# Kernel tuning notes

Measured on AMD Instinct MI355X. Metric: run time of the kernel, lower is better.

## Reference

```python
import jax, jax.numpy as jnp
import numpy as np

B, N, C, H, HD, HH, WW, K, ALPHA = 8, 4096, 256, 8, 32, 64, 64, 5, 4.0


def setup_inputs() -> dict:
    key = jax.random.key(0)
    ks = jax.random.split(key, 6)
    return {
        "x": jax.random.normal(ks[0], (B, N, C), jnp.float32),
        "W_qg": jax.random.normal(ks[1], (C, 2 * C), jnp.float32) * 0.02,
        "W_kv": jax.random.normal(ks[2], (C, 2 * C), jnp.float32) * 0.02,
        "W_proj": jax.random.normal(ks[3], (C, C), jnp.float32) * 0.02,
        "b_proj": jnp.zeros((C,), jnp.float32),
        "dwc_w": jax.random.normal(ks[4], (HD, 1, K, K), jnp.float32) * 0.05,
        "dwc_b": jnp.zeros((HD,), jnp.float32),
        "power_p": jnp.zeros((1, H, 1, HD), jnp.float32),
    }


def _safe_pow(x, p):
    # x >= 0 (post-relu). 0**p == 0 for p > 0; guard base so grads stay finite.
    xs = jnp.where(x > 0, x, 1.0)
    return jnp.where(x > 0, xs ** p, 0.0)


def reference(x, W_qg, W_kv, W_proj, b_proj, dwc_w, dwc_b, power_p):
    qg = x @ W_qg                                  # (B,N,2C)
    q, g = qg[..., :C], qg[..., C:]
    kv = x @ W_kv                                  # (B,N,2C)
    k = kv[..., :C].reshape(B, N, H, HD).transpose(0, 2, 1, 3)   # (B,H,N,hd)
    v = kv[..., C:].reshape(B, N, H, HD).transpose(0, 2, 1, 3)
    q = q.reshape(B, N, H, HD).transpose(0, 2, 1, 3)

    power = 1.0 + ALPHA * jax.nn.sigmoid(power_p)  # (1,H,1,hd)
    # x_s = q_pos@kv_s + q_neg@kv_s = (q_pos+q_neg)@kv_s, kv_s = (k_pos+k_neg)^T v_s
    q_sum = _safe_pow(jax.nn.relu(q), power) + _safe_pow(jax.nn.relu(-q), power)
    k_sum = _safe_pow(jax.nn.relu(k), power) + _safe_pow(jax.nn.relu(-k), power)

    v_s, v_o = v[..., : HD // 2], v[..., HD // 2 :]
    kv_s = jnp.einsum('bhnd,bhne->bhde', k_sum, v_s)
    kv_o = jnp.einsum('bhnd,bhne->bhde', k_sum, v_o)
    x_s = jnp.einsum('bhnd,bhde->bhne', q_sum, kv_s)
    x_o = jnp.einsum('bhnd,bhde->bhne', q_sum, kv_o)
    x_att = jnp.concatenate([x_s, x_o], -1).transpose(0, 2, 1, 3).reshape(B, N, C)

    # depthwise conv branch: exact layout replication of torch permute/reshape chain
    v_img = v.transpose(0, 2, 1, 3).reshape(B * H, HD, HH, WW)
    pad = K // 2
    v_loc = jax.lax.conv_general_dilated(
        v_img, dwc_w, (1, 1), [(pad, pad), (pad, pad)],
        feature_group_count=HD,
        dimension_numbers=('NCHW', 'OIHW', 'NCHW')) + dwc_b[None, :, None, None]
    v_loc = v_loc.reshape(B, H, HD, N).transpose(0, 2, 1, 3).reshape(B, C, N).transpose(0, 2, 1)

    return ((x_att + v_loc) * g) @ W_proj + b_proj
```

## Files before the change

kernel.cpp:

```cpp
#include <hip/hip_runtime.h>
#include <hip/hip_bf16.h>
#include <math.h>

#define B_ 8
#define N_ 4096
#define C_ 256
#define H_ 8
#define HD_ 32
#define BN_ (B_ * N_)
#define E_ ((size_t)BN_ * C_)

typedef __attribute__((ext_vector_type(8))) short short8;
typedef __attribute__((ext_vector_type(4))) float f32x4;

__device__ __forceinline__ float b2f(__hip_bfloat16 x) { return __bfloat162float(x); }

__device__ __forceinline__ void gl_lds16(const void* gp, void* lp) {
    __builtin_amdgcn_global_load_lds(
        (const __attribute__((address_space(1))) unsigned int*)gp,
        (__attribute__((address_space(3))) unsigned int*)lp,
        16, 0, 0);
}

__device__ __forceinline__ float fast_abspow(float v, float p) {
    float av = fabsf(v);
    return (av > 0.f) ? exp2f(p * __log2f(av)) : 0.f;
}

__device__ __forceinline__ float bf_lo(unsigned u) { return __uint_as_float(u << 16); }
__device__ __forceinline__ float bf_hi(unsigned u) { return __uint_as_float(u & 0xffff0000u); }
__device__ __forceinline__ unsigned short f2bfbits(float f) {
    __hip_bfloat16 h = __float2bfloat16(f);
    return *(unsigned short*)&h;
}

__global__ __launch_bounds__(256) void cvt_all(
    const float* __restrict__ x, const float* __restrict__ Wqg,
    const float* __restrict__ Wkv, const float* __restrict__ Wp,
    const float* __restrict__ pp,
    __hip_bfloat16* __restrict__ xb, __hip_bfloat16* __restrict__ Wt1,
    __hip_bfloat16* __restrict__ Wt2, float* __restrict__ powers)
{
    int t = threadIdx.x;
    int bid0 = blockIdx.x;
    if (bid0 < 8192) {
        size_t i = ((size_t)bid0 * 256 + t) * 4;
        float4 v = *(const float4*)&x[i];
        xb[i + 0] = __float2bfloat16(v.x);
        xb[i + 1] = __float2bfloat16(v.y);
        xb[i + 2] = __float2bfloat16(v.z);
        xb[i + 3] = __float2bfloat16(v.w);
        return;
    }
    int bid = bid0 - 8192;
    if (bid == 80) {
        powers[t] = 1.0f + 4.0f / (1.0f + expf(-pp[t]));
        return;
    }
    __shared__ float tile[64][65];
    const float* src;
    __hip_bfloat16* dst;
    int scols, tr, tc, dn0;
    if (bid < 32)      { src = Wqg; scols = 512; tr = bid >> 3;        tc = bid & 7;        dst = Wt1; dn0 = tc * 64; }
    else if (bid < 64) { src = Wkv; scols = 512; tr = (bid - 32) >> 3; tc = (bid - 32) & 7; dst = Wt1; dn0 = 512 + tc * 64; }
    else               { src = Wp;  scols = 256; tr = (bid - 64) >> 2; tc = (bid - 64) & 3; dst = Wt2; dn0 = tc * 64; }
    int tx = t & 63, ty = t >> 6;
    #pragma unroll
    for (int i = 0; i < 16; i++) {
        int r = ty + i * 4;
        tile[r][tx] = src[(size_t)(tr * 64 + r) * scols + tc * 64 + tx];
    }
    __syncthreads();
    #pragma unroll
    for (int i = 0; i < 16; i++) {
        int n_local = ty + i * 4;
        dst[(size_t)(dn0 + n_local) * 256 + tr * 64 + tx] = __float2bfloat16(tile[tx][n_local]);
    }
}

__global__ __launch_bounds__(256) void gemm1_mfma(
    const __hip_bfloat16* __restrict__ xb, const __hip_bfloat16* __restrict__ Wt1,
    const float* __restrict__ powers,
    __hip_bfloat16* __restrict__ q16, __hip_bfloat16* __restrict__ k16,
    __hip_bfloat16* __restrict__ g16, __hip_bfloat16* __restrict__ v16)
{
    __shared__ __align__(16) unsigned short As[2 * 128 * 32];
    __shared__ __align__(16) unsigned short Bs[2 * 128 * 32];
    int t = threadIdx.x;
    int w = t >> 6, l = t & 63;
    int row0 = blockIdx.x * 128;
    int col0 = blockIdx.y * 128;
    int wm = (w >> 1) * 64, wn = (w & 1) * 64;
    int lane15 = l & 15, quad = l >> 4;
    int srow = l >> 2;
    int skcol = (l & 3) * 8;

    f32x4 acc[4][4];
    #pragma unroll
    for (int mi = 0; mi < 4; mi++)
        #pragma unroll
        for (int ni = 0; ni < 4; ni++) acc[mi][ni] = (f32x4){0.f, 0.f, 0.f, 0.f};

    for (int k0 = 0; k0 < 256; k0 += 64) {
        #pragma unroll
        for (int kh = 0; kh < 2; kh++) {
            #pragma unroll
            for (int i = 0; i < 2; i++) {
                int r = i * 64 + w * 16 + srow;
                int kc = k0 + kh * 32 + skcol;
                gl_lds16(&xb[(size_t)(row0 + r) * 256 + kc],
                         &As[kh * 4096 + (i * 64 + w * 16) * 32]);
                gl_lds16(&Wt1[(size_t)(col0 + r) * 256 + kc],
                         &Bs[kh * 4096 + (i * 64 + w * 16) * 32]);
            }
        }
        __syncthreads();
        #pragma unroll
        for (int kh = 0; kh < 2; kh++) {
            short8 a[4], b[4];
            #pragma unroll
            for (int mi = 0; mi < 4; mi++)
                a[mi] = *(const short8*)&As[kh * 4096 + (wm + mi * 16 + lane15) * 32 + quad * 8];
            #pragma unroll
            for (int ni = 0; ni < 4; ni++)
                b[ni] = *(const short8*)&Bs[kh * 4096 + (wn + ni * 16 + lane15) * 32 + quad * 8];
            #pragma unroll
            for (int mi = 0; mi < 4; mi++)
                #pragma unroll
                for (int ni = 0; ni < 4; ni++)
                    acc[mi][ni] = __builtin_amdgcn_mfma_f32_16x16x32_bf16(a[mi], b[ni], acc[mi][ni], 0, 0, 0);
        }
        __syncthreads();
    }

    int region = blockIdx.y >> 1;
    #pragma unroll
    for (int mi = 0; mi < 4; mi++) {
        #pragma unroll
        for (int ni = 0; ni < 4; ni++) {
            int row = row0 + wm + mi * 16 + quad * 4;
            int col = col0 + wn + ni * 16 + lane15;
            int c255 = col & 255;
            float p = powers[c255];
            #pragma unroll
            for (int r = 0; r < 4; r++) {
                float v = acc[mi][ni][r];
                size_t idx = (size_t)(row + r) * 256 + c255;
                if (region == 0) {
                    q16[idx] = __float2bfloat16(fast_abspow(v, p));
                } else if (region == 1) {
                    g16[idx] = __float2bfloat16(v);
                } else if (region == 2) {
                    k16[idx] = __float2bfloat16(fast_abspow(v, p));
                } else {
                    v16[idx] = __float2bfloat16(v);
                }
            }
        }
    }
}

__global__ __launch_bounds__(256) void kvmat_kernel(
    const __hip_bfloat16* __restrict__ k16, const __hip_bfloat16* __restrict__ v16,
    float* __restrict__ kv_part)
{
    __shared__ __align__(16) unsigned short Kl[16 * 256];
    __shared__ __align__(16) unsigned short Vl[16 * 256];
    int t = threadIdx.x;
    int bid = blockIdx.x;
    int b = bid >> 5, seg = bid & 31;
    int h = t >> 5;
    float acc[32];
    #pragma unroll
    for (int e = 0; e < 32; e++) acc[e] = 0.f;
    const size_t base = (size_t)b * N_ * 256;
    int row = t >> 4, colb = (t & 15) * 16;
    for (int n0 = seg * 128; n0 < seg * 128 + 128; n0 += 16) {
        const uint4* ks = (const uint4*)(k16 + base + (size_t)(n0 + row) * 256 + colb);
        uint4 ka = ks[0], kb = ks[1];
        const uint4* vs = (const uint4*)(v16 + base + (size_t)(n0 + row) * 256 + colb);
        uint4 va = vs[0], vb = vs[1];
        __syncthreads();
        uint4* kd4 = (uint4*)&Kl[row * 256 + colb];
        kd4[0] = ka; kd4[1] = kb;
        uint4* vd4 = (uint4*)&Vl[row * 256 + colb];
        vd4[0] = va; vd4[1] = vb;
        __syncthreads();
        #pragma unroll
        for (int nn = 0; nn < 16; nn++) {
            unsigned short ku = Kl[nn * 256 + t];
            float kd = bf_lo((unsigned)ku);
            const uint4* vp = (const uint4*)&Vl[nn * 256 + h * 32];
            uint4 v0 = vp[0], v1 = vp[1], v2 = vp[2], v3 = vp[3];
            unsigned us[16] = {v0.x, v0.y, v0.z, v0.w, v1.x, v1.y, v1.z, v1.w,
                               v2.x, v2.y, v2.z, v2.w, v3.x, v3.y, v3.z, v3.w};
            #pragma unroll
            for (int j = 0; j < 16; j++) {
                acc[2 * j]     += kd * bf_lo(us[j]);
                acc[2 * j + 1] += kd * bf_hi(us[j]);
            }
        }
    }
    float* dst = kv_part + (size_t)bid * 8192;
    #pragma unroll
    for (int e = 0; e < 32; e++) dst[e * 256 + t] = acc[e];
}

__global__ __launch_bounds__(256) void kv_reduce(
    const float* __restrict__ kv_part, float* __restrict__ kv_mat2)
{
    int bid = blockIdx.x, t = threadIdx.x;
    int b = bid >> 3, chunk = bid & 7;
    #pragma unroll
    for (int j = 0; j < 4; j++) {
        int i = chunk * 1024 + j * 256 + t;
        float s = 0.f;
        for (int seg = 0; seg < 32; seg++)
            s += kv_part[((size_t)b * 32 + seg) * 8192 + i];
        kv_mat2[(size_t)b * 8192 + i] = s;
    }
}

__global__ __launch_bounds__(256) void conv_kernel(
    const __hip_bfloat16* __restrict__ v16,
    const float* __restrict__ w, const float* __restrict__ bias,
    __hip_bfloat16* __restrict__ vloc)
{
    __shared__ __align__(16) float img[64 * 72];
    __shared__ float wl[25];
    int t = threadIdx.x;
    int gid = blockIdx.x;
    int DD = gid & 31;
    if (t < 128) {
        int row = t >> 1, side = (t & 1) * 68;
        *(float4*)&img[row * 72 + side] = (float4){0.f, 0.f, 0.f, 0.f};
    }
    if (t < 25) wl[t] = w[DD * 25 + t];
    {
        int row = t >> 2, colb = (t & 3) * 16;
        const uint4* src = (const uint4*)(v16 + (size_t)gid * 4096 + row * 64 + colb);
        uint4 u0 = src[0], u1 = src[1];
        float4* d = (float4*)&img[row * 72 + 4 + colb];
        d[0] = (float4){bf_lo(u0.x), bf_hi(u0.x), bf_lo(u0.y), bf_hi(u0.y)};
        d[1] = (float4){bf_lo(u0.z), bf_hi(u0.z), bf_lo(u0.w), bf_hi(u0.w)};
        d[2] = (float4){bf_lo(u1.x), bf_hi(u1.x), bf_lo(u1.y), bf_hi(u1.y)};
        d[3] = (float4){bf_lo(u1.z), bf_hi(u1.z), bf_lo(u1.w), bf_hi(u1.w)};
    }
    __syncthreads();
    float bs = bias[DD];
    int x0 = (t & 15) * 4, yb = t >> 4;
    #pragma unroll
    for (int s = 0; s < 4; s++) {
        int y = yb + s * 16;
        float a0 = bs, a1 = bs, a2 = bs, a3 = bs;
        #pragma unroll
        for (int ky = 0; ky < 5; ky++) {
            int row = y + ky - 2;
            if (row < 0 || row >= 64) continue;
            const float* rp = &img[row * 72 + x0];
            float4 w0 = *(const float4*)rp;
            float4 w1 = *(const float4*)(rp + 4);
            float4 w2 = *(const float4*)(rp + 8);
            float win[12] = {w0.x, w0.y, w0.z, w0.w, w1.x, w1.y, w1.z, w1.w,
                             w2.x, w2.y, w2.z, w2.w};
            #pragma unroll
            for (int kx = 0; kx < 5; kx++) {
                float wt = wl[ky * 5 + kx];
                a0 += wt * win[2 + kx];
                a1 += wt * win[3 + kx];
                a2 += wt * win[4 + kx];
                a3 += wt * win[5 + kx];
            }
        }
        unsigned lo = (unsigned)f2bfbits(a0) | ((unsigned)f2bfbits(a1) << 16);
        unsigned hi = (unsigned)f2bfbits(a2) | ((unsigned)f2bfbits(a3) << 16);
        *(uint2*)(vloc + (size_t)gid * 4096 + y * 64 + x0) = (uint2){lo, hi};
    }
}

#define A2P 264
__global__ __launch_bounds__(256) void att_gemm2(
    const __hip_bfloat16* __restrict__ q16, const float* __restrict__ kv_mat2,
    const __hip_bfloat16* __restrict__ vloc, const __hip_bfloat16* __restrict__ g16,
    const __hip_bfloat16* __restrict__ Wt2, const float* __restrict__ bp,
    float* __restrict__ out)
{
    __shared__ __align__(16) unsigned short QA[64 * A2P];
    __shared__ __align__(16) unsigned short Bs[256 * 32];
    int t = threadIdx.x;
    int w = t >> 6, l = t & 63;
    int r0 = blockIdx.x * 64;
    int b = r0 >> 12, n0 = r0 & 4095;
    int lane15 = l & 15, quad = l >> 4;
    int h0 = w * 2;

    {
        const uint4* qsrc = (const uint4*)(q16 + (size_t)(r0 + (t >> 2)) * 256 + (t & 3) * 64);
        uint4* qdst = (uint4*)&QA[(t >> 2) * A2P + (t & 3) * 64];
        #pragma unroll
        for (int j = 0; j < 8; j++) qdst[j] = qsrc[j];
    }
    __syncthreads();

    short8 afr[4][2];
    #pragma unroll
    for (int m = 0; m < 4; m++)
        #pragma unroll
        for (int hh = 0; hh < 2; hh++)
            afr[m][hh] = *(const short8*)&QA[(m * 16 + lane15) * A2P + (h0 + hh) * 32 + quad * 8];

    short8 bfr[2][2];
    #pragma unroll
    for (int hh = 0; hh < 2; hh++) {
        #pragma unroll
        for (int nt = 0; nt < 2; nt++) {
            const float4* kp = (const float4*)(kv_mat2 + (size_t)b * 8192 +
                (size_t)(nt * 16 + lane15) * 256 + (h0 + hh) * 32 + quad * 8);
            float4 ka = kp[0], kb = kp[1];
            short8 bb;
            bb[0] = (short)f2bfbits(ka.x); bb[1] = (short)f2bfbits(ka.y);
            bb[2] = (short)f2bfbits(ka.z); bb[3] = (short)f2bfbits(ka.w);
            bb[4] = (short)f2bfbits(kb.x); bb[5] = (short)f2bfbits(kb.y);
            bb[6] = (short)f2bfbits(kb.z); bb[7] = (short)f2bfbits(kb.w);
            bfr[hh][nt] = bb;
        }
    }

    f32x4 ac[4][2][2];
    #pragma unroll
    for (int m = 0; m < 4; m++)
        #pragma unroll
        for (int hh = 0; hh < 2; hh++)
            #pragma unroll
            for (int nt = 0; nt < 2; nt++)
                ac[m][hh][nt] = __builtin_amdgcn_mfma_f32_16x16x32_bf16(
                    afr[m][hh], bfr[hh][nt], (f32x4){0.f, 0.f, 0.f, 0.f}, 0, 0, 0);

    #pragma unroll
    for (int m = 0; m < 4; m++) {
        #pragma unroll
        for (int hh = 0; hh < 2; hh++) {
            #pragma unroll
            for (int nt = 0; nt < 2; nt++) {
                int col = (h0 + hh) * 32 + nt * 16 + lane15;
                int rowb = m * 16 + quad * 4;
                size_t img = ((size_t)((b * 8 + (col & 7)) * 32 + (col >> 3))) * 4096 + n0 + rowb;
                uint2 vv = *(const uint2*)(vloc + img);
                float vl[4] = {bf_lo(vv.x), bf_hi(vv.x), bf_lo(vv.y), bf_hi(vv.y)};
                #pragma unroll
                for (int i = 0; i < 4; i++) {
                    float gg = b2f(g16[(size_t)(r0 + rowb + i) * 256 + col]);
                    float val = (ac[m][hh][nt][i] + vl[i]) * gg;
                    QA[(rowb + i) * A2P + col] = f2bfbits(val);
                }
            }
        }
    }

    int wm = (w & 1) * 32, wn = (w >> 1) * 128;
    f32x4 acc2[2][8];
    #pragma unroll
    for (int mi = 0; mi < 2; mi++)
        #pragma unroll
        for (int ni = 0; ni < 8; ni++) acc2[mi][ni] = (f32x4){0.f, 0.f, 0.f, 0.f};

    for (int k0 = 0; k0 < 256; k0 += 32) {
        __syncthreads();
        #pragma unroll
        for (int i = 0; i < 4; i++) {
            int ncol = i * 64 + w * 16 + (l >> 2);
            gl_lds16(&Wt2[(size_t)ncol * 256 + k0 + (l & 3) * 8],
                     &Bs[(i * 64 + w * 16) * 32]);
        }
        __syncthreads();
        short8 a[2], bb[8];
        #pragma unroll
        for (int mi = 0; mi < 2; mi++)
            a[mi] = *(const short8*)&QA[(wm + mi * 16 + lane15) * A2P + k0 + quad * 8];
        #pragma unroll
        for (int ni = 0; ni < 8; ni++)
            bb[ni] = *(const short8*)&Bs[(wn + ni * 16 + lane15) * 32 + quad * 8];
        #pragma unroll
        for (int mi = 0; mi < 2; mi++)
            #pragma unroll
            for (int ni = 0; ni < 8; ni++)
                acc2[mi][ni] = __builtin_amdgcn_mfma_f32_16x16x32_bf16(a[mi], bb[ni], acc2[mi][ni], 0, 0, 0);
    }

    #pragma unroll
    for (int mi = 0; mi < 2; mi++) {
        #pragma unroll
        for (int ni = 0; ni < 8; ni++) {
            int row = r0 + wm + mi * 16 + quad * 4;
            int col = wn + ni * 16 + lane15;
            float bv = bp[col];
            #pragma unroll
            for (int r = 0; r < 4; r++)
                out[(size_t)(row + r) * 256 + col] = acc2[mi][ni][r] + bv;
        }
    }
}

extern "C" void kernel_launch(void* const* d_in, const int* in_sizes, int n_in,
                              void* d_out, int out_size, void* d_ws, size_t ws_size,
                              hipStream_t stream) {
    const float* x      = (const float*)d_in[0];
    const float* W_qg   = (const float*)d_in[1];
    const float* W_kv   = (const float*)d_in[2];
    const float* W_proj = (const float*)d_in[3];
    const float* b_proj = (const float*)d_in[4];
    const float* dwc_w  = (const float*)d_in[5];
    const float* dwc_b  = (const float*)d_in[6];
    const float* pow_p  = (const float*)d_in[7];
    float* out = (float*)d_out;

    float* ws = (float*)d_ws;
    const size_t E = E_;
    __hip_bfloat16* q16  = (__hip_bfloat16*)ws;
    __hip_bfloat16* k16  = (__hip_bfloat16*)(ws + E / 2);
    __hip_bfloat16* vl16 = k16;
    __hip_bfloat16* g16  = (__hip_bfloat16*)(ws + E);
    __hip_bfloat16* v16  = (__hip_bfloat16*)(ws + 3 * E / 2);
    __hip_bfloat16* xb   = (__hip_bfloat16*)(ws + 2 * E);
    float* kv_part = ws + 5 * E / 2;
    float* kv_mat2 = kv_part + 256 * 8192;
    __hip_bfloat16* Wt1 = (__hip_bfloat16*)(kv_mat2 + 65536);
    __hip_bfloat16* Wt2 = Wt1 + 262144;
    float* powers = (float*)(Wt2 + 65536);

    cvt_all<<<8192 + 81, 256, 0, stream>>>(x, W_qg, W_kv, W_proj, pow_p, xb, Wt1, Wt2, powers);
    gemm1_mfma<<<dim3(BN_ / 128, 8), 256, 0, stream>>>(xb, Wt1, powers, q16, k16, g16, v16);
    kvmat_kernel<<<256, 256, 0, stream>>>(k16, v16, kv_part);
    kv_reduce<<<64, 256, 0, stream>>>(kv_part, kv_mat2);
    conv_kernel<<<2048, 256, 0, stream>>>(v16, dwc_w, dwc_b, vl16);
    att_gemm2<<<512, 256, 0, stream>>>(q16, kv_mat2, vl16, g16, Wt2, b_proj, out);
}
```

Before: 206.6 us.

## Stage GEMM1 epilogue through LDS and fuse kv-matrix, reduction and conv kernels

The GEMM1 epilogue now writes results into a padded shared-memory tile and then stores them to global memory as coalesced 16-byte rows, replacing scattered 2-byte stores. The kv-matrix kernel, kv reduction kernel and depthwise conv kernel are merged into one launch with heterogeneous blocks. Partial kv sums are combined with float atomicAdd into a buffer zeroed by a memset, which removes the separate reduction pass. The conv output moves to its own workspace region because k16 is still being read concurrently, and the atomics make the float summation order nondeterministic.

```diff
diff --git a/kernel.cpp b/kernel.cpp
--- a/kernel.cpp
+++ b/kernel.cpp
@@ -78,14 +78,16 @@
     }
 }
 
+#define EP 132
 __global__ __launch_bounds__(256) void gemm1_mfma(
     const __hip_bfloat16* __restrict__ xb, const __hip_bfloat16* __restrict__ Wt1,
     const float* __restrict__ powers,
     __hip_bfloat16* __restrict__ q16, __hip_bfloat16* __restrict__ k16,
     __hip_bfloat16* __restrict__ g16, __hip_bfloat16* __restrict__ v16)
 {
-    __shared__ __align__(16) unsigned short As[2 * 128 * 32];
-    __shared__ __align__(16) unsigned short Bs[2 * 128 * 32];
+    __shared__ __align__(16) unsigned short SMEM[128 * EP];
+    unsigned short* As = SMEM;
+    unsigned short* Bs = SMEM + 8192;
     int t = threadIdx.x;
     int w = t >> 6, l = t & 63;
     int row0 = blockIdx.x * 128;
@@ -134,147 +136,129 @@
     }
 
     int region = blockIdx.y >> 1;
+    bool dopow = (region == 0) || (region == 2);
     #pragma unroll
     for (int mi = 0; mi < 4; mi++) {
         #pragma unroll
         for (int ni = 0; ni < 4; ni++) {
-            int row = row0 + wm + mi * 16 + quad * 4;
-            int col = col0 + wn + ni * 16 + lane15;
-            int c255 = col & 255;
-            float p = powers[c255];
+            int lrow = wm + mi * 16 + quad * 4;
+            int lcol = wn + ni * 16 + lane15;
+            float p = powers[(col0 + lcol) & 255];
             #pragma unroll
             for (int r = 0; r < 4; r++) {
                 float v = acc[mi][ni][r];
-                size_t idx = (size_t)(row + r) * 256 + c255;
-                if (region == 0) {
-                    q16[idx] = __float2bfloat16(fast_abspow(v, p));
-                } else if (region == 1) {
-                    g16[idx] = __float2bfloat16(v);
-                } else if (region == 2) {
-                    k16[idx] = __float2bfloat16(fast_abspow(v, p));
-                } else {
-                    v16[idx] = __float2bfloat16(v);
-                }
+                float o = dopow ? fast_abspow(v, p) : v;
+                SMEM[(lrow + r) * EP + lcol] = f2bfbits(o);
             }
         }
     }
-}
-
-__global__ __launch_bounds__(256) void kvmat_kernel(
+    __syncthreads();
+    __hip_bfloat16* dst = (region == 0) ? q16 : (region == 1) ? g16 : (region == 2) ? k16 : v16;
+    int sr = t >> 1, sc = (t & 1) * 64;
+    const unsigned short* src = &SMEM[sr * EP + sc];
+    __hip_bfloat16* gp = dst + (size_t)(row0 + sr) * 256 + ((col0 + sc) & 255);
+    #pragma unroll
+    for (int j = 0; j < 8; j++)
+        *(uint4*)(gp + j * 8) = *(const uint4*)(src + j * 8);
+}
+
+__global__ __launch_bounds__(256) void kvmat_conv(
     const __hip_bfloat16* __restrict__ k16, const __hip_bfloat16* __restrict__ v16,
-    float* __restrict__ kv_part)
-{
-    __shared__ __align__(16) unsigned short Kl[16 * 256];
-    __shared__ __align__(16) unsigned short Vl[16 * 256];
-    int t = threadIdx.x;
-    int bid = blockIdx.x;
-    int b = bid >> 5, seg = bid & 31;
-    int h = t >> 5;
-    float acc[32];
-    #pragma unroll
-    for (int e = 0; e < 32; e++) acc[e] = 0.f;
-    const size_t base = (size_t)b * N_ * 256;
-    int row = t >> 4, colb = (t & 15) * 16;
-    for (int n0 = seg * 128; n0 < seg * 128 + 128; n0 += 16) {
-        const uint4* ks = (const uint4*)(k16 + base + (size_t)(n0 + row) * 256 + colb);
-        uint4 ka = ks[0], kb = ks[1];
-        const uint4* vs = (const uint4*)(v16 + base + (size_t)(n0 + row) * 256 + colb);
-        uint4 va = vs[0], vb = vs[1];
-        __syncthreads();
-        uint4* kd4 = (uint4*)&Kl[row * 256 + colb];
-        kd4[0] = ka; kd4[1] = kb;
-        uint4* vd4 = (uint4*)&Vl[row * 256 + colb];
-        vd4[0] = va; vd4[1] = vb;
-        __syncthreads();
-        #pragma unroll
-        for (int nn = 0; nn < 16; nn++) {
-            unsigned short ku = Kl[nn * 256 + t];
-            float kd = bf_lo((unsigned)ku);
-            const uint4* vp = (const uint4*)&Vl[nn * 256 + h * 32];
-            uint4 v0 = vp[0], v1 = vp[1], v2 = vp[2], v3 = vp[3];
-            unsigned us[16] = {v0.x, v0.y, v0.z, v0.w, v1.x, v1.y, v1.z, v1.w,
-                               v2.x, v2.y, v2.z, v2.w, v3.x, v3.y, v3.z, v3.w};
-            #pragma unroll
-            for (int j = 0; j < 16; j++) {
-                acc[2 * j]     += kd * bf_lo(us[j]);
-                acc[2 * j + 1] += kd * bf_hi(us[j]);
-            }
-        }
-    }
-    float* dst = kv_part + (size_t)bid * 8192;
-    #pragma unroll
-    for (int e = 0; e < 32; e++) dst[e * 256 + t] = acc[e];
-}
-
-__global__ __launch_bounds__(256) void kv_reduce(
-    const float* __restrict__ kv_part, float* __restrict__ kv_mat2)
-{
-    int bid = blockIdx.x, t = threadIdx.x;
-    int b = bid >> 3, chunk = bid & 7;
-    #pragma unroll
-    for (int j = 0; j < 4; j++) {
-        int i = chunk * 1024 + j * 256 + t;
-        float s = 0.f;
-        for (int seg = 0; seg < 32; seg++)
-            s += kv_part[((size_t)b * 32 + seg) * 8192 + i];
-        kv_mat2[(size_t)b * 8192 + i] = s;
-    }
-}
-
-__global__ __launch_bounds__(256) void conv_kernel(
-    const __hip_bfloat16* __restrict__ v16,
+    float* __restrict__ kv_mat2,
     const float* __restrict__ w, const float* __restrict__ bias,
     __hip_bfloat16* __restrict__ vloc)
 {
-    __shared__ __align__(16) float img[64 * 72];
-    __shared__ float wl[25];
+    __shared__ __align__(16) float SM[4640];
     int t = threadIdx.x;
-    int gid = blockIdx.x;
-    int DD = gid & 31;
-    if (t < 128) {
-        int row = t >> 1, side = (t & 1) * 68;
-        *(float4*)&img[row * 72 + side] = (float4){0.f, 0.f, 0.f, 0.f};
-    }
-    if (t < 25) wl[t] = w[DD * 25 + t];
-    {
-        int row = t >> 2, colb = (t & 3) * 16;
-        const uint4* src = (const uint4*)(v16 + (size_t)gid * 4096 + row * 64 + colb);
-        uint4 u0 = src[0], u1 = src[1];
-        float4* d = (float4*)&img[row * 72 + 4 + colb];
-        d[0] = (float4){bf_lo(u0.x), bf_hi(u0.x), bf_lo(u0.y), bf_hi(u0.y)};
-        d[1] = (float4){bf_lo(u0.z), bf_hi(u0.z), bf_lo(u0.w), bf_hi(u0.w)};
-        d[2] = (float4){bf_lo(u1.x), bf_hi(u1.x), bf_lo(u1.y), bf_hi(u1.y)};
-        d[3] = (float4){bf_lo(u1.z), bf_hi(u1.z), bf_lo(u1.w), bf_hi(u1.w)};
-    }
-    __syncthreads();
-    float bs = bias[DD];
-    int x0 = (t & 15) * 4, yb = t >> 4;
-    #pragma unroll
-    for (int s = 0; s < 4; s++) {
-        int y = yb + s * 16;
-        float a0 = bs, a1 = bs, a2 = bs, a3 = bs;
-        #pragma unroll
-        for (int ky = 0; ky < 5; ky++) {
-            int row = y + ky - 2;
-            if (row < 0 || row >= 64) continue;
-            const float* rp = &img[row * 72 + x0];
-            float4 w0 = *(const float4*)rp;
-            float4 w1 = *(const float4*)(rp + 4);
-            float4 w2 = *(const float4*)(rp + 8);
-            float win[12] = {w0.x, w0.y, w0.z, w0.w, w1.x, w1.y, w1.z, w1.w,
-                             w2.x, w2.y, w2.z, w2.w};
-            #pragma unroll
-            for (int kx = 0; kx < 5; kx++) {
-                float wt = wl[ky * 5 + kx];
-                a0 += wt * win[2 + kx];
-                a1 += wt * win[3 + kx];
-                a2 += wt * win[4 + kx];
-                a3 += wt * win[5 + kx];
+    int bid = blockIdx.x;
+    if (bid < 256) {
+        unsigned short* Kl = (unsigned short*)SM;
+        unsigned short* Vl = (unsigned short*)SM + 4096;
+        int b = bid >> 5, seg = bid & 31;
+        int h = t >> 5;
+        float acc[32];
+        #pragma unroll
+        for (int e = 0; e < 32; e++) acc[e] = 0.f;
+        const size_t base = (size_t)b * N_ * 256;
+        int row = t >> 4, colb = (t & 15) * 16;
+        for (int n0 = seg * 128; n0 < seg * 128 + 128; n0 += 16) {
+            const uint4* ks = (const uint4*)(k16 + base + (size_t)(n0 + row) * 256 + colb);
+            uint4 ka = ks[0], kb = ks[1];
+            const uint4* vs = (const uint4*)(v16 + base + (size_t)(n0 + row) * 256 + colb);
+            uint4 va = vs[0], vb = vs[1];
+            __syncthreads();
+            uint4* kd4 = (uint4*)&Kl[row * 256 + colb];
+            kd4[0] = ka; kd4[1] = kb;
+            uint4* vd4 = (uint4*)&Vl[row * 256 + colb];
+            vd4[0] = va; vd4[1] = vb;
+            __syncthreads();
+            #pragma unroll
+            for (int nn = 0; nn < 16; nn++) {
+                float kd = bf_lo((unsigned)Kl[nn * 256 + t]);
+                const uint4* vp = (const uint4*)&Vl[nn * 256 + h * 32];
+                uint4 v0 = vp[0], v1 = vp[1], v2 = vp[2], v3 = vp[3];
+                unsigned us[16] = {v0.x, v0.y, v0.z, v0.w, v1.x, v1.y, v1.z, v1.w,
+                                   v2.x, v2.y, v2.z, v2.w, v3.x, v3.y, v3.z, v3.w};
+                #pragma unroll
+                for (int j = 0; j < 16; j++) {
+                    acc[2 * j]     += kd * bf_lo(us[j]);
+                    acc[2 * j + 1] += kd * bf_hi(us[j]);
+                }
             }
         }
-        unsigned lo = (unsigned)f2bfbits(a0) | ((unsigned)f2bfbits(a1) << 16);
-        unsigned hi = (unsigned)f2bfbits(a2) | ((unsigned)f2bfbits(a3) << 16);
-        *(uint2*)(vloc + (size_t)gid * 4096 + y * 64 + x0) = (uint2){lo, hi};
+        float* dst = kv_mat2 + (size_t)b * 8192;
+        #pragma unroll
+        for (int e = 0; e < 32; e++) atomicAdd(&dst[e * 256 + t], acc[e]);
+    } else {
+        float* img = SM;
+        float* wl  = SM + 4608;
+        int gid = bid - 256;
+        int DD = gid & 31;
+        if (t < 128) {
+            int row = t >> 1, side = (t & 1) * 68;
+            *(float4*)&img[row * 72 + side] = (float4){0.f, 0.f, 0.f, 0.f};
+        }
+        if (t < 25) wl[t] = w[DD * 25 + t];
+        {
+            int row = t >> 2, colb = (t & 3) * 16;
+            const uint4* src = (const uint4*)(v16 + (size_t)gid * 4096 + row * 64 + colb);
+            uint4 u0 = src[0], u1 = src[1];
+            float4* d = (float4*)&img[row * 72 + 4 + colb];
+            d[0] = (float4){bf_lo(u0.x), bf_hi(u0.x), bf_lo(u0.y), bf_hi(u0.y)};
+            d[1] = (float4){bf_lo(u0.z), bf_hi(u0.z), bf_lo(u0.w), bf_hi(u0.w)};
+            d[2] = (float4){bf_lo(u1.x), bf_hi(u1.x), bf_lo(u1.y), bf_hi(u1.y)};
+            d[3] = (float4){bf_lo(u1.z), bf_hi(u1.z), bf_lo(u1.w), bf_hi(u1.w)};
+        }
+        __syncthreads();
+        float bs = bias[DD];
+        int x0 = (t & 15) * 4, yb = t >> 4;
+        #pragma unroll
+        for (int s = 0; s < 4; s++) {
+            int y = yb + s * 16;
+            float a0 = bs, a1 = bs, a2 = bs, a3 = bs;
+            #pragma unroll
+            for (int ky = 0; ky < 5; ky++) {
+                int row = y + ky - 2;
+                if (row < 0 || row >= 64) continue;
+                const float* rp = &img[row * 72 + x0];
+                float4 w0 = *(const float4*)rp;
+                float4 w1 = *(const float4*)(rp + 4);
+                float4 w2 = *(const float4*)(rp + 8);
+                float win[12] = {w0.x, w0.y, w0.z, w0.w, w1.x, w1.y, w1.z, w1.w,
+                                 w2.x, w2.y, w2.z, w2.w};
+                #pragma unroll
+                for (int kx = 0; kx < 5; kx++) {
+                    float wt = wl[ky * 5 + kx];
+                    a0 += wt * win[2 + kx];
+                    a1 += wt * win[3 + kx];
+                    a2 += wt * win[4 + kx];
+                    a3 += wt * win[5 + kx];
+                }
+            }
+            unsigned lo = (unsigned)f2bfbits(a0) | ((unsigned)f2bfbits(a1) << 16);
+            unsigned hi = (unsigned)f2bfbits(a2) | ((unsigned)f2bfbits(a3) << 16);
+            *(uint2*)(vloc + (size_t)gid * 4096 + y * 64 + x0) = (uint2){lo, hi};
+        }
     }
 }
 
@@ -418,20 +402,18 @@
     const size_t E = E_;
     __hip_bfloat16* q16  = (__hip_bfloat16*)ws;
     __hip_bfloat16* k16  = (__hip_bfloat16*)(ws + E / 2);
-    __hip_bfloat16* vl16 = k16;
     __hip_bfloat16* g16  = (__hip_bfloat16*)(ws + E);
     __hip_bfloat16* v16  = (__hip_bfloat16*)(ws + 3 * E / 2);
     __hip_bfloat16* xb   = (__hip_bfloat16*)(ws + 2 * E);
-    float* kv_part = ws + 5 * E / 2;
-    float* kv_mat2 = kv_part + 256 * 8192;
+    __hip_bfloat16* vl16 = (__hip_bfloat16*)(ws + 5 * E / 2);
+    float* kv_mat2 = ws + 3 * E;
     __hip_bfloat16* Wt1 = (__hip_bfloat16*)(kv_mat2 + 65536);
     __hip_bfloat16* Wt2 = Wt1 + 262144;
     float* powers = (float*)(Wt2 + 65536);
 
+    hipMemsetAsync(kv_mat2, 0, 65536 * sizeof(float), stream);
     cvt_all<<<8192 + 81, 256, 0, stream>>>(x, W_qg, W_kv, W_proj, pow_p, xb, Wt1, Wt2, powers);
     gemm1_mfma<<<dim3(BN_ / 128, 8), 256, 0, stream>>>(xb, Wt1, powers, q16, k16, g16, v16);
-    kvmat_kernel<<<256, 256, 0, stream>>>(k16, v16, kv_part);
-    kv_reduce<<<64, 256, 0, stream>>>(kv_part, kv_mat2);
-    conv_kernel<<<2048, 256, 0, stream>>>(v16, dwc_w, dwc_b, vl16);
+    kvmat_conv<<<256 + 2048, 256, 0, stream>>>(k16, v16, kv_mat2, dwc_w, dwc_b, vl16);
     att_gemm2<<<512, 256, 0, stream>>>(q16, kv_mat2, vl16, g16, Wt2, b_proj, out);
 }
```

After: 224.8 us. 8.8% more time.
